# Optimization experiments

Measured on AMD Instinct MI355X. Metric: run time of the kernel, lower is better.

Reference implementation:

```python
import jax, jax.numpy as jnp
import numpy as np

N_HEADS = 32
N_KV_HEADS = 8
THETA = 10000.0


def _rope_tables(head_dim, seq_len):
    # freqs: [head_dim//2]
    freqs = 1.0 / (THETA ** (jnp.arange(0, head_dim, 2, dtype=jnp.float32) / head_dim))
    ang = jnp.arange(seq_len, dtype=jnp.float32)[:, None] * freqs[None, :]  # [T, hd/2]
    return jnp.cos(ang), jnp.sin(ang)


def _apply_rope(x, cos, sin):
    # x: [B, T, H, hd]; cos/sin: [T, hd/2] -> broadcast [1, T, 1, hd/2]
    x_even = x[..., 0::2]
    x_odd = x[..., 1::2]
    c = cos[None, :, None, :]
    s = sin[None, :, None, :]
    out_even = x_even * c - x_odd * s
    out_odd = x_even * s + x_odd * c
    # interleave back to [..., hd]
    out = jnp.stack([out_even, out_odd], axis=-1)
    return out.reshape(x.shape)


def setup_inputs() -> dict:
    key = jax.random.key(0)
    ks = jax.random.split(key, 5)
    B, T, C = 2, 2048, 2048
    kv_dim = (C // N_HEADS) * N_KV_HEADS  # 512
    sc = 1.0 / np.sqrt(C)
    return {
        "x": jax.random.normal(ks[0], (B, T, C), dtype=jnp.float32),
        "wq": jax.random.normal(ks[1], (C, C), dtype=jnp.float32) * sc,
        "wk": jax.random.normal(ks[2], (C, kv_dim), dtype=jnp.float32) * sc,
        "wv": jax.random.normal(ks[3], (C, kv_dim), dtype=jnp.float32) * sc,
        "wo": jax.random.normal(ks[4], (C, C), dtype=jnp.float32) * sc,
    }


def reference(x, wq, wk, wv, wo):
    B, T, C = x.shape
    hd = C // N_HEADS
    rep = N_HEADS // N_KV_HEADS

    q = (x @ wq).reshape(B, T, N_HEADS, hd)
    k = (x @ wk).reshape(B, T, N_KV_HEADS, hd)
    v = (x @ wv).reshape(B, T, N_KV_HEADS, hd)

    cos, sin = _rope_tables(hd, T)
    q = _apply_rope(q, cos, sin)
    k = _apply_rope(k, cos, sin)

    q = q.transpose(0, 2, 1, 3)  # [B, H, T, hd]
    k = k.transpose(0, 2, 1, 3)  # [B, KV, T, hd]
    v = v.transpose(0, 2, 1, 3)

    # GQA: repeat_interleave kv heads to match q heads
    k = jnp.repeat(k, rep, axis=1)
    v = jnp.repeat(v, rep, axis=1)

    scores = jnp.einsum("bhtd,bhsd->bhts", q, k) / jnp.sqrt(jnp.float32(hd))
    weights = jax.nn.softmax(scores, axis=-1)  # no causal mask, as in source
    out = jnp.einsum("bhts,bhsd->bhtd", weights, v)
    out = out.transpose(0, 2, 1, 3).reshape(B, T, C)
    return out @ wo
```

## Files before the change

### kernel.cpp

```cpp
#include <hip/hip_runtime.h>
#include <hip/hip_bf16.h>


typedef unsigned short u16;
typedef short bf16x8 __attribute__((ext_vector_type(8)));
typedef float f32x4 __attribute__((ext_vector_type(4)));
typedef unsigned uint32x4 __attribute__((ext_vector_type(4)));

#define LOG2E 1.4426950408889634f
#define NFREQ (-13.287712379549449f / 32.f)

#if __has_builtin(__builtin_amdgcn_exp2f)
#define EXP2F(x) __builtin_amdgcn_exp2f(x)
#else
#define EXP2F(x) exp2f(x)
#endif

__device__ __forceinline__ float bf2f(u16 u) {
    union { unsigned v; float f; } x; x.v = ((unsigned)u) << 16; return x.f;
}
__device__ __forceinline__ u16 f2bf(float f) {
    unsigned u = __float_as_uint(f);
    u += 0x7fffu + ((u >> 16) & 1u);
    return (u16)(u >> 16);
}
__device__ __forceinline__ unsigned cvt_pk_bf16(float lo, float hi) {
    unsigned r;
    asm("v_cvt_pk_bf16_f32 %0, %1, %2" : "=v"(r) : "v"(lo), "v"(hi));
    return r;
}

__device__ __forceinline__ void async_copy16(const void* g, void* l) {
    __builtin_amdgcn_global_load_lds((const __attribute__((address_space(1))) void*)g,
                                     (__attribute__((address_space(3))) void*)l, 16, 0, 0);
}

#define MFMA16(d, a, b) d = __builtin_amdgcn_mfma_f32_16x16x32_bf16(a, b, d, 0, 0, 0)

__global__ void prep_kernel(const float* __restrict__ x,
                            const float* __restrict__ wq, const float* __restrict__ wk,
                            const float* __restrict__ wv, const float* __restrict__ wo,
                            u16* __restrict__ xbf, u16* __restrict__ wqkvT,
                            u16* __restrict__ woT, float2* __restrict__ rtab) {
    const int bz = blockIdx.z;
    if (bz < 4) {
        const int K = 2048;
        const float* W; u16* Wt; int N;
        switch (bz) {
            case 0:  W = wq; Wt = wqkvT;                        N = 2048; break;
            case 1:  W = wk; Wt = wqkvT + (size_t)2048 * 2048;  N = 512;  break;
            case 2:  W = wv; Wt = wqkvT + (size_t)2560 * 2048;  N = 512;  break;
            default: W = wo; Wt = woT;                          N = 2048; break;
        }
        if ((int)blockIdx.x * 32 >= N) return;
        __shared__ float tile[32][33];
        int xx = blockIdx.x * 32 + threadIdx.x;
        int y0 = blockIdx.y * 32 + threadIdx.y;
        #pragma unroll
        for (int r = 0; r < 32; r += 8)
            tile[threadIdx.y + r][threadIdx.x] = W[(size_t)(y0 + r) * N + xx];
        __syncthreads();
        int xo = blockIdx.y * 32 + threadIdx.x;
        int yo0 = blockIdx.x * 32 + threadIdx.y;
        #pragma unroll
        for (int r = 0; r < 32; r += 8)
            Wt[(size_t)(yo0 + r) * K + xo] = f2bf(tile[threadIdx.x][threadIdx.y + r]);
    } else if (bz == 4) {
        int bid = blockIdx.y * gridDim.x + blockIdx.x;
        int tid = threadIdx.y * 32 + threadIdx.x;
        const size_t n4 = (size_t)4096 * 2048 / 4;
        for (size_t i = (size_t)bid * 256 + tid; i < n4; i += (size_t)4096 * 256) {
            float4 v = ((const float4*)x)[i];
            ushort4 o;
            o.x = f2bf(v.x); o.y = f2bf(v.y); o.z = f2bf(v.z); o.w = f2bf(v.w);
            ((ushort4*)xbf)[i] = o;
        }
    } else {
        int bid = blockIdx.y * gridDim.x + blockIdx.x;
        int idx = bid * 256 + threadIdx.y * 32 + threadIdx.x;
        if (idx < 2048 * 32) {
            int t = idx >> 5, i = idx & 31;
            float freq = exp2f((float)i * NFREQ);
            float s, c;
            sincosf((float)t * freq, &s, &c);
            rtab[idx] = make_float2(c, s);
        }
    }
}

__global__ __launch_bounds__(512) void gemm_qkv_kernel(const u16* __restrict__ A,
                                                       const u16* __restrict__ Bt,
                                                       u16* __restrict__ qout,
                                                       u16* __restrict__ kout,
                                                       u16* __restrict__ vtout,
                                                       const float2* __restrict__ rope_tab,
                                                       int N, int K) {
    __shared__ __align__(16) u16 As[2][16384];
    __shared__ __align__(16) u16 Bs[2][16384];

    const int tid = threadIdx.x;
    const int nwgx = N >> 8;
    const int nwg = 16 * nwgx;
    const int wg = blockIdx.x;
    const int swz = (wg & 7) * (nwg >> 3) + (wg >> 3);
    const int m0 = (swz / nwgx) << 8;
    const int n0 = (swz % nwgx) << 8;

    const int w = tid >> 6, lane = tid & 63, quad = lane >> 4, ln = lane & 15;
    const int wm = w >> 2, wn = w & 3;

    int ldo[2], r128[2], cg8[2];
    #pragma unroll
    for (int p = 0; p < 2; p++) {
        int chunk = p * 512 + tid;
        r128[p] = chunk >> 3;
        cg8[p] = ((chunk & 7) ^ ((chunk >> 3) & 7)) << 3;
        ldo[p] = chunk << 3;
    }
    const u16* pA[2][2]; const u16* pB[2][2];
    #pragma unroll
    for (int h = 0; h < 2; h++)
        #pragma unroll
        for (int p = 0; p < 2; p++) {
            pA[h][p] = A  + (size_t)(m0 + h * 128 + r128[p]) * K + cg8[p];
            pB[h][p] = Bt + (size_t)(n0 + h * 128 + r128[p]) * K + cg8[p];
        }

#define STAGE_A(h, buf) { async_copy16(pA[h][0], &As[buf][(h) * 8192 + ldo[0]]); pA[h][0] += 64; \
                          async_copy16(pA[h][1], &As[buf][(h) * 8192 + ldo[1]]); pA[h][1] += 64; }
#define STAGE_B(h, buf) { async_copy16(pB[h][0], &Bs[buf][(h) * 8192 + ldo[0]]); pB[h][0] += 64; \
                          async_copy16(pB[h][1], &Bs[buf][(h) * 8192 + ldo[1]]); pB[h][1] += 64; }

    f32x4 acc[2][2][4][2];
    #pragma unroll
    for (int mh = 0; mh < 2; mh++)
        #pragma unroll
        for (int nh = 0; nh < 2; nh++)
            #pragma unroll
            for (int i = 0; i < 4; i++)
                #pragma unroll
                for (int j = 0; j < 2; j++)
                    acc[mh][nh][i][j] = (f32x4){0.f, 0.f, 0.f, 0.f};

    STAGE_A(0, 0); STAGE_B(0, 0); STAGE_B(1, 0); STAGE_A(1, 0);
    asm volatile("s_waitcnt vmcnt(4)" ::: "memory");
    __builtin_amdgcn_s_barrier();

    const int nt = K >> 6;
    bf16x8 a[2][4], b0[2][2], b1[2][2];
    const int clq0 = quad ^ (ln & 7), clq1 = (4 + quad) ^ (ln & 7);

    for (int t = 0; t < nt - 1; ++t) {
        const int cur = t & 1, nxt = cur ^ 1;
        const u16* AsC = As[cur];
        const u16* BsC = Bs[cur];
        #pragma unroll
        for (int i = 0; i < 4; i++) {
            int r = wm * 64 + i * 16 + ln;
            a[0][i] = *(const bf16x8*)(&AsC[r * 64 + clq0 * 8]);
            a[1][i] = *(const bf16x8*)(&AsC[r * 64 + clq1 * 8]);
        }
        #pragma unroll
        for (int j = 0; j < 2; j++) {
            int r = wn * 32 + j * 16 + ln;
            b0[0][j] = *(const bf16x8*)(&BsC[r * 64 + clq0 * 8]);
            b0[1][j] = *(const bf16x8*)(&BsC[r * 64 + clq1 * 8]);
        }
        STAGE_A(0, nxt);
        asm volatile("s_waitcnt vmcnt(4)" ::: "memory");
        __builtin_amdgcn_s_barrier();
        __builtin_amdgcn_s_setprio(1);
        #pragma unroll
        for (int kk = 0; kk < 2; kk++)
            #pragma unroll
            for (int i = 0; i < 4; i++)
                #pragma unroll
                for (int j = 0; j < 2; j++)
                    MFMA16(acc[0][0][i][j], a[kk][i], b0[kk][j]);
        __builtin_amdgcn_s_setprio(0);
        __builtin_amdgcn_s_barrier();
        #pragma unroll
        for (int j = 0; j < 2; j++) {
            int r = 128 + wn * 32 + j * 16 + ln;
            b1[0][j] = *(const bf16x8*)(&BsC[r * 64 + clq0 * 8]);
            b1[1][j] = *(const bf16x8*)(&BsC[r * 64 + clq1 * 8]);
        }
        STAGE_B(0, nxt);
        asm volatile("s_waitcnt vmcnt(4)" ::: "memory");
        __builtin_amdgcn_s_barrier();
        __builtin_amdgcn_s_setprio(1);
        #pragma unroll
        for (int kk = 0; kk < 2; kk++)
            #pragma unroll
            for (int i = 0; i < 4; i++)
                #pragma unroll
                for (int j = 0; j < 2; j++)
                    MFMA16(acc[0][1][i][j], a[kk][i], b1[kk][j]);
        __builtin_amdgcn_s_setprio(0);
        __builtin_amdgcn_s_barrier();
        #pragma unroll
        for (int i = 0; i < 4; i++) {
            int r = 128 + wm * 64 + i * 16 + ln;
            a[0][i] = *(const bf16x8*)(&AsC[r * 64 + clq0 * 8]);
            a[1][i] = *(const bf16x8*)(&AsC[r * 64 + clq1 * 8]);
        }
        STAGE_B(1, nxt);
        asm volatile("s_waitcnt vmcnt(4)" ::: "memory");
        __builtin_amdgcn_s_barrier();
        __builtin_amdgcn_s_setprio(1);
        #pragma unroll
        for (int kk = 0; kk < 2; kk++)
            #pragma unroll
            for (int i = 0; i < 4; i++)
                #pragma unroll
                for (int j = 0; j < 2; j++)
                    MFMA16(acc[1][0][i][j], a[kk][i], b0[kk][j]);
        __builtin_amdgcn_s_setprio(0);
        __builtin_amdgcn_s_barrier();
        STAGE_A(1, nxt);
        asm volatile("s_waitcnt vmcnt(4)" ::: "memory");
        __builtin_amdgcn_s_barrier();
        __builtin_amdgcn_s_setprio(1);
        #pragma unroll
        for (int kk = 0; kk < 2; kk++)
            #pragma unroll
            for (int i = 0; i < 4; i++)
                #pragma unroll
                for (int j = 0; j < 2; j++)
                    MFMA16(acc[1][1][i][j], a[kk][i], b1[kk][j]);
        __builtin_amdgcn_s_setprio(0);
        __builtin_amdgcn_s_barrier();
    }

    asm volatile("s_waitcnt vmcnt(0)" ::: "memory");
    __builtin_amdgcn_s_barrier();
    {
        const u16* AsC = As[(nt - 1) & 1];
        const u16* BsC = Bs[(nt - 1) & 1];
        #pragma unroll
        for (int mh = 0; mh < 2; mh++) {
            #pragma unroll
            for (int i = 0; i < 4; i++) {
                int r = mh * 128 + wm * 64 + i * 16 + ln;
                a[0][i] = *(const bf16x8*)(&AsC[r * 64 + clq0 * 8]);
                a[1][i] = *(const bf16x8*)(&AsC[r * 64 + clq1 * 8]);
            }
            #pragma unroll
            for (int nh = 0; nh < 2; nh++) {
                bf16x8 bb[2][2];
                #pragma unroll
                for (int j = 0; j < 2; j++) {
                    int r = nh * 128 + wn * 32 + j * 16 + ln;
                    bb[0][j] = *(const bf16x8*)(&BsC[r * 64 + clq0 * 8]);
                    bb[1][j] = *(const bf16x8*)(&BsC[r * 64 + clq1 * 8]);
                }
                #pragma unroll
                for (int kk = 0; kk < 2; kk++)
                    #pragma unroll
                    for (int i = 0; i < 4; i++)
                        #pragma unroll
                        for (int j = 0; j < 2; j++)
                            MFMA16(acc[mh][nh][i][j], a[kk][i], bb[kk][j]);
            }
        }
    }
#undef STAGE_A
#undef STAGE_B

    if (n0 >= 2560) {
        #pragma unroll
        for (int mh = 0; mh < 2; mh++)
            #pragma unroll
            for (int i = 0; i < 4; i++) {
                int cb = mh * 128 + wm * 64 + i * 16 + quad * 4;
                int sp = (cb & 128) | (cb & 96) | ((cb & 12) << 1) | ((cb & 16) >> 2);
                #pragma unroll
                for (int nh = 0; nh < 2; nh++)
                    #pragma unroll
                    for (int j = 0; j < 2; j++) {
                        int d = n0 + nh * 128 + wn * 32 + j * 16 + ln - 2560;
                        ushort4 o;
                        o.x = f2bf(acc[mh][nh][i][j][0]); o.y = f2bf(acc[mh][nh][i][j][1]);
                        o.z = f2bf(acc[mh][nh][i][j][2]); o.w = f2bf(acc[mh][nh][i][j][3]);
                        *(ushort4*)(&vtout[(size_t)d * 4096 + m0 + sp]) = o;
                    }
            }
        return;
    }
    u16* dst; int ldc, coff; float scale = 1.f;
    if (n0 < 2048) { dst = qout; ldc = 2048; coff = 0;    scale = 0.125f * LOG2E; }
    else           { dst = kout; ldc = 512;  coff = 2048; }
    float fsin = (ln & 1) ? 1.f : -1.f;
    #pragma unroll
    for (int mh = 0; mh < 2; mh++)
        #pragma unroll
        for (int i = 0; i < 4; i++)
            #pragma unroll
            for (int rr = 0; rr < 4; rr++) {
                int row = m0 + mh * 128 + wm * 64 + i * 16 + quad * 4 + rr;
                const float2* trow = rope_tab + (size_t)(row & 2047) * 32;
                #pragma unroll
                for (int nh = 0; nh < 2; nh++)
                    #pragma unroll
                    for (int j = 0; j < 2; j++) {
                        int col = n0 + nh * 128 + wn * 32 + j * 16 + ln;
                        float v = acc[mh][nh][i][j][rr];
                        float p = __shfl_xor(v, 1, 64);
                        float2 cs = trow[(col & 63) >> 1];
                        float rr2 = (v * cs.x + fsin * p * cs.y) * scale;
                        dst[(size_t)row * ldc + col - coff] = f2bf(rr2);
                    }
            }
}

__global__ __launch_bounds__(512) void gemm_out_kernel(const u16* __restrict__ A,
                                                       const u16* __restrict__ Bt,
                                                       float* __restrict__ fC,
                                                       int N, int K) {
    __shared__ __align__(16) u16 As[2][16384];
    __shared__ __align__(16) u16 Bs[2][8192];

    const int tid = threadIdx.x;
    const int nbx = N >> 7;
    const int nwg = 16 * nbx;
    const int wg = blockIdx.x;
    const int swz = (wg & 7) * (nwg >> 3) + (wg >> 3);
    const int m0 = (swz / nbx) << 8;
    const int n0 = (swz % nbx) << 7;

    const int w = tid >> 6, lane = tid & 63, quad = lane >> 4, ln = lane & 15;
    const int wm = w >> 2, wn = w & 3;

    int ldoA[2], rA[2], cgA[2];
    #pragma unroll
    for (int p = 0; p < 2; p++) {
        int chunk = p * 512 + tid;
        rA[p] = chunk >> 3;
        cgA[p] = ((chunk & 7) ^ ((chunk >> 3) & 7)) << 3;
        ldoA[p] = chunk << 3;
    }
    const int rB = tid >> 3;
    const int cgB = ((tid & 7) ^ (rB & 7)) << 3;
    const int ldoB = tid << 3;

    const u16* pA[2][2]; const u16* pB[2];
    #pragma unroll
    for (int h = 0; h < 2; h++) {
        #pragma unroll
        for (int p = 0; p < 2; p++)
            pA[h][p] = A + (size_t)(m0 + h * 128 + rA[p]) * K + cgA[p];
        pB[h] = Bt + (size_t)(n0 + h * 64 + rB) * K + cgB;
    }

#define STAGE_A(h, buf) { async_copy16(pA[h][0], &As[buf][(h) * 8192 + ldoA[0]]); pA[h][0] += 64; \
                          async_copy16(pA[h][1], &As[buf][(h) * 8192 + ldoA[1]]); pA[h][1] += 64; }
#define STAGE_B(h, buf) { async_copy16(pB[h], &Bs[buf][(h) * 4096 + ldoB]); pB[h] += 64; }

    f32x4 acc[2][2][4];
    #pragma unroll
    for (int mh = 0; mh < 2; mh++)
        #pragma unroll
        for (int nh = 0; nh < 2; nh++)
            #pragma unroll
            for (int i = 0; i < 4; i++)
                acc[mh][nh][i] = (f32x4){0.f, 0.f, 0.f, 0.f};

    STAGE_A(0, 0); STAGE_B(0, 0); STAGE_B(1, 0); STAGE_A(1, 0);
    asm volatile("s_waitcnt vmcnt(3)" ::: "memory");
    __builtin_amdgcn_s_barrier();

    const int nt = K >> 6;
    bf16x8 a[2][4], bb0[2], bb1[2];
    const int clq0 = quad ^ (ln & 7), clq1 = (4 + quad) ^ (ln & 7);

    for (int t = 0; t < nt - 1; ++t) {
        const int cur = t & 1, nxt = cur ^ 1;
        const u16* AsC = As[cur];
        const u16* BsC = Bs[cur];
        #pragma unroll
        for (int i = 0; i < 4; i++) {
            int r = wm * 64 + i * 16 + ln;
            a[0][i] = *(const bf16x8*)(&AsC[r * 64 + clq0 * 8]);
            a[1][i] = *(const bf16x8*)(&AsC[r * 64 + clq1 * 8]);
        }
        {
            int r = wn * 16 + ln;
            bb0[0] = *(const bf16x8*)(&BsC[r * 64 + clq0 * 8]);
            bb0[1] = *(const bf16x8*)(&BsC[r * 64 + clq1 * 8]);
        }
        STAGE_A(0, nxt);
        asm volatile("s_waitcnt vmcnt(4)" ::: "memory");
        __builtin_amdgcn_s_barrier();
        __builtin_amdgcn_s_setprio(1);
        #pragma unroll
        for (int kk = 0; kk < 2; kk++)
            #pragma unroll
            for (int i = 0; i < 4; i++)
                MFMA16(acc[0][0][i], a[kk][i], bb0[kk]);
        __builtin_amdgcn_s_setprio(0);
        __builtin_amdgcn_s_barrier();
        {
            int r = wn * 16 + ln;
            bb1[0] = *(const bf16x8*)(&BsC[4096 + r * 64 + clq0 * 8]);
            bb1[1] = *(const bf16x8*)(&BsC[4096 + r * 64 + clq1 * 8]);
        }
        STAGE_B(0, nxt);
        asm volatile("s_waitcnt vmcnt(3)" ::: "memory");
        __builtin_amdgcn_s_barrier();
        __builtin_amdgcn_s_setprio(1);
        #pragma unroll
        for (int kk = 0; kk < 2; kk++)
            #pragma unroll
            for (int i = 0; i < 4; i++)
                MFMA16(acc[0][1][i], a[kk][i], bb1[kk]);
        __builtin_amdgcn_s_setprio(0);
        __builtin_amdgcn_s_barrier();
        #pragma unroll
        for (int i = 0; i < 4; i++) {
            int r = 128 + wm * 64 + i * 16 + ln;
            a[0][i] = *(const bf16x8*)(&AsC[r * 64 + clq0 * 8]);
            a[1][i] = *(const bf16x8*)(&AsC[r * 64 + clq1 * 8]);
        }
        STAGE_B(1, nxt);
        asm volatile("s_waitcnt vmcnt(4)" ::: "memory");
        __builtin_amdgcn_s_barrier();
        __builtin_amdgcn_s_setprio(1);
        #pragma unroll
        for (int kk = 0; kk < 2; kk++)
            #pragma unroll
            for (int i = 0; i < 4; i++)
                MFMA16(acc[1][0][i], a[kk][i], bb0[kk]);
        __builtin_amdgcn_s_setprio(0);
        __builtin_amdgcn_s_barrier();
        STAGE_A(1, nxt);
        asm volatile("s_waitcnt vmcnt(3)" ::: "memory");
        __builtin_amdgcn_s_barrier();
        __builtin_amdgcn_s_setprio(1);
        #pragma unroll
        for (int kk = 0; kk < 2; kk++)
            #pragma unroll
            for (int i = 0; i < 4; i++)
                MFMA16(acc[1][1][i], a[kk][i], bb1[kk]);
        __builtin_amdgcn_s_setprio(0);
        __builtin_amdgcn_s_barrier();
    }

    asm volatile("s_waitcnt vmcnt(0)" ::: "memory");
    __builtin_amdgcn_s_barrier();
    {
        const u16* AsC = As[(nt - 1) & 1];
        const u16* BsC = Bs[(nt - 1) & 1];
        #pragma unroll
        for (int mh = 0; mh < 2; mh++) {
            #pragma unroll
            for (int i = 0; i < 4; i++) {
                int r = mh * 128 + wm * 64 + i * 16 + ln;
                a[0][i] = *(const bf16x8*)(&AsC[r * 64 + clq0 * 8]);
                a[1][i] = *(const bf16x8*)(&AsC[r * 64 + clq1 * 8]);
            }
            #pragma unroll
            for (int nh = 0; nh < 2; nh++) {
                bf16x8 bb[2];
                int r = wn * 16 + ln;
                bb[0] = *(const bf16x8*)(&BsC[nh * 4096 + r * 64 + clq0 * 8]);
                bb[1] = *(const bf16x8*)(&BsC[nh * 4096 + r * 64 + clq1 * 8]);
                #pragma unroll
                for (int kk = 0; kk < 2; kk++)
                    #pragma unroll
                    for (int i = 0; i < 4; i++)
                        MFMA16(acc[mh][nh][i], a[kk][i], bb[kk]);
            }
        }
    }
#undef STAGE_A
#undef STAGE_B

    #pragma unroll
    for (int mh = 0; mh < 2; mh++)
        #pragma unroll
        for (int i = 0; i < 4; i++)
            #pragma unroll
            for (int rr = 0; rr < 4; rr++) {
                int row = m0 + mh * 128 + wm * 64 + i * 16 + quad * 4 + rr;
                #pragma unroll
                for (int nh = 0; nh < 2; nh++) {
                    int col = n0 + nh * 64 + wn * 16 + ln;
                    fC[(size_t)row * N + col] = acc[mh][nh][i][rr];
                }
            }
}

__global__ __launch_bounds__(256) void attn_kernel(const u16* __restrict__ qb,
                                                   const u16* __restrict__ kb,
                                                   const u16* __restrict__ vtb,
                                                   u16* __restrict__ ob) {
    const int T = 2048;
    const int CQ = 2048, CKV = 512;
    __shared__ __align__(16) u16 Ks[2][128 * 64];
    __shared__ __align__(16) u16 Vt[2][64 * 128];

    const int tid = threadIdx.x;
    const int bh = blockIdx.y;
    const int b = bh >> 5, h = bh & 31, kvh = h >> 2;
    const int t0 = blockIdx.x * 128;
    const u16* qbase = qb + ((size_t)(b * T + t0) * CQ + h * 64);
    const u16* kbase = kb + ((size_t)(b * T) * CKV + kvh * 64);
    const u16* vtbase = vtb + ((size_t)(kvh * 64)) * 4096 + b * 2048;

    const int w = tid >> 6, lane = tid & 63, quad = lane >> 4, ln = lane & 15;

    bf16x8 ones;
    #pragma unroll
    for (int e = 0; e < 8; e++) ones[e] = (short)0x3F80;

    const u16* kp[4]; const u16* vp[4];
    int chunks[4];
    #pragma unroll
    for (int p = 0; p < 4; p++) {
        int chunk = p * 256 + tid;
        chunks[p] = chunk;
        int r = chunk >> 3, cl = chunk & 7;
        int cg = cl ^ (r & 7);
        kp[p] = kbase + (size_t)r * CKV + cg * 8;
        int d = chunk >> 4, cl2 = chunk & 15;
        int cg2 = cl2 ^ (d & 7);
        vp[p] = vtbase + (size_t)d * 4096 + cg2 * 8;
    }

    bf16x8 qf[2][2];
    #pragma unroll
    for (int i = 0; i < 2; i++)
        #pragma unroll
        for (int kk = 0; kk < 2; kk++)
            qf[i][kk] = *(const bf16x8*)(&qbase[(size_t)(w * 32 + i * 16 + ln) * CQ + kk * 32 + quad * 8]);

    f32x4 o_acc[2][4];
    f32x4 l_acc[2];
    #pragma unroll
    for (int i = 0; i < 2; i++) {
        l_acc[i] = (f32x4){0.f, 0.f, 0.f, 0.f};
        #pragma unroll
        for (int j = 0; j < 4; j++) o_acc[i][j] = (f32x4){0.f, 0.f, 0.f, 0.f};
    }
    const f32x4 zero4 = (f32x4){0.f, 0.f, 0.f, 0.f};

    #pragma unroll
    for (int p = 0; p < 4; p++) {
        async_copy16(kp[p], &Ks[0][chunks[p] * 8]);
        async_copy16(vp[p], &Vt[0][chunks[p] * 8]);
        kp[p] += 128 * CKV;
        vp[p] += 128;
    }
    __syncthreads();

    int cur = 0;
    for (int st = 0; st < T; st += 128) {
        if (st + 128 < T) {
            #pragma unroll
            for (int p = 0; p < 4; p++) {
                async_copy16(kp[p], &Ks[cur ^ 1][chunks[p] * 8]);
                async_copy16(vp[p], &Vt[cur ^ 1][chunks[p] * 8]);
                kp[p] += 128 * CKV;
                vp[p] += 128;
            }
        }
        const u16* KsC = Ks[cur];
        const u16* VtC = Vt[cur];

        f32x4 s_acc[8][2];
        {
            bf16x8 kf[8];
            #pragma unroll
            for (int j = 0; j < 8; j++) {
                int r = j * 16 + ln;
                int cl = quad ^ (ln & 7);
                kf[j] = *(const bf16x8*)(&KsC[r * 64 + cl * 8]);
            }
            __builtin_amdgcn_s_setprio(1);
            #pragma unroll
            for (int j = 0; j < 8; j++)
                #pragma unroll
                for (int i = 0; i < 2; i++)
                    s_acc[j][i] = __builtin_amdgcn_mfma_f32_16x16x32_bf16(kf[j], qf[i][0], zero4, 0, 0, 0);
            __builtin_amdgcn_s_setprio(0);
        }
        {
            bf16x8 kf[8];
            #pragma unroll
            for (int j = 0; j < 8; j++) {
                int r = j * 16 + ln;
                int cl = (4 + quad) ^ (ln & 7);
                kf[j] = *(const bf16x8*)(&KsC[r * 64 + cl * 8]);
            }
            __builtin_amdgcn_s_setprio(1);
            #pragma unroll
            for (int j = 0; j < 8; j++)
                #pragma unroll
                for (int i = 0; i < 2; i++)
                    s_acc[j][i] = __builtin_amdgcn_mfma_f32_16x16x32_bf16(kf[j], qf[i][1], s_acc[j][i], 0, 0, 0);
            __builtin_amdgcn_s_setprio(0);
        }

        bf16x8 pa[2][4];
        #pragma unroll
        for (int i = 0; i < 2; i++)
            #pragma unroll
            for (int c = 0; c < 4; c++) {
                unsigned w0 = cvt_pk_bf16(EXP2F(s_acc[2 * c][i][0]),     EXP2F(s_acc[2 * c][i][1]));
                unsigned w1 = cvt_pk_bf16(EXP2F(s_acc[2 * c][i][2]),     EXP2F(s_acc[2 * c][i][3]));
                unsigned w2 = cvt_pk_bf16(EXP2F(s_acc[2 * c + 1][i][0]), EXP2F(s_acc[2 * c + 1][i][1]));
                unsigned w3 = cvt_pk_bf16(EXP2F(s_acc[2 * c + 1][i][2]), EXP2F(s_acc[2 * c + 1][i][3]));
                union { uint32x4 u; bf16x8 b; } pu;
                pu.u = (uint32x4){w0, w1, w2, w3};
                pa[i][c] = pu.b;
            }

        #pragma unroll
        for (int c = 0; c < 4; c++) {
            bf16x8 vb[4];
            #pragma unroll
            for (int jd = 0; jd < 4; jd++) {
                int d = jd * 16 + ln;
                int cg = c * 4 + quad;
                int cl = (cg & 8) | ((cg ^ (d & 7)) & 7);
                vb[jd] = *(const bf16x8*)(&VtC[d * 128 + cl * 8]);
            }
            __builtin_amdgcn_s_setprio(1);
            #pragma unroll
            for (int i = 0; i < 2; i++) {
                l_acc[i] = __builtin_amdgcn_mfma_f32_16x16x32_bf16(pa[i][c], ones, l_acc[i], 0, 0, 0);
                #pragma unroll
                for (int jd = 0; jd < 4; jd++)
                    o_acc[i][jd] = __builtin_amdgcn_mfma_f32_16x16x32_bf16(pa[i][c], vb[jd], o_acc[i][jd], 0, 0, 0);
            }
            __builtin_amdgcn_s_setprio(0);
        }

        __syncthreads();
        cur ^= 1;
    }

    #pragma unroll
    for (int i = 0; i < 2; i++)
        #pragma unroll
        for (int rr = 0; rr < 4; rr++) {
            float linv = 1.f / l_acc[i][rr];
            int row = w * 32 + i * 16 + quad * 4 + rr;
            #pragma unroll
            for (int jd = 0; jd < 4; jd++) {
                int col = jd * 16 + ln;
                ob[(size_t)(b * T + t0 + row) * CQ + h * 64 + col] = f2bf(o_acc[i][jd][rr] * linv);
            }
        }
}

#define WS_X_BF   ((size_t)0)
#define WS_WQKVT  ((size_t)16777216)
#define WS_WOT    ((size_t)29360128)
#define WS_QBF    ((size_t)37748736)
#define WS_KBF    ((size_t)54525952)
#define WS_VTBF   ((size_t)58720256)
#define WS_ABF    ((size_t)62914560)

extern "C" void kernel_launch(void* const* d_in, const int* in_sizes, int n_in,
                              void* d_out, int out_size, void* d_ws, size_t ws_size,
                              hipStream_t stream) {
    const float* x  = (const float*)d_in[0];
    const float* wq = (const float*)d_in[1];
    const float* wk = (const float*)d_in[2];
    const float* wv = (const float*)d_in[3];
    const float* wo = (const float*)d_in[4];
    char* ws = (char*)d_ws;
    u16* xbf   = (u16*)(ws + WS_X_BF);
    u16* wqkvT = (u16*)(ws + WS_WQKVT);
    u16* woT   = (u16*)(ws + WS_WOT);
    u16* qbf   = (u16*)(ws + WS_QBF);
    u16* kbf   = (u16*)(ws + WS_KBF);
    u16* vtbf  = (u16*)(ws + WS_VTBF);
    u16* abf   = (u16*)(ws + WS_ABF);
    float2* rtab = (float2*)(ws + WS_ABF);
    float* out = (float*)d_out;

    prep_kernel<<<dim3(64, 64, 6), dim3(32, 8), 0, stream>>>(x, wq, wk, wv, wo,
                                                             xbf, wqkvT, woT, rtab);

    gemm_qkv_kernel<<<dim3(192), 512, 0, stream>>>(xbf, wqkvT, qbf, kbf, vtbf, rtab,
                                                   3072, 2048);

    attn_kernel<<<dim3(16, 64), 256, 0, stream>>>(qbf, kbf, vtbf, abf);

    gemm_out_kernel<<<dim3(256), 512, 0, stream>>>(abf, woT, out, 2048, 2048);
}
```

Before: 289.5 us.

## Widen attention query tile to 256 rows and vectorize weight transpose

The attention kernel now runs 512 threads (8 waves) per block and covers 256 query rows instead of 128. Each double-buffered K/V tile is therefore shared by twice as many queries, which halves global K/V traffic per query, but the grid shrinks to 512 blocks. The prep kernel's weight transpose moves to 64x64 tiles that read with float4 loads, convert to bf16 before staging in shared memory, and write ushort4 vectors. The prep grid is shrunk to match, and the x-conversion loop stride is adjusted to the new block count.

```diff
diff --git a/kernel.cpp b/kernel.cpp
--- a/kernel.cpp
+++ b/kernel.cpp
@@ -43,6 +43,7 @@
                             u16* __restrict__ xbf, u16* __restrict__ wqkvT,
                             u16* __restrict__ woT, float2* __restrict__ rtab) {
     const int bz = blockIdx.z;
+    const int tid = threadIdx.y * 32 + threadIdx.x;
     if (bz < 4) {
         const int K = 2048;
         const float* W; u16* Wt; int N;
@@ -52,24 +53,32 @@
             case 2:  W = wv; Wt = wqkvT + (size_t)2560 * 2048;  N = 512;  break;
             default: W = wo; Wt = woT;                          N = 2048; break;
         }
-        if ((int)blockIdx.x * 32 >= N) return;
-        __shared__ float tile[32][33];
-        int xx = blockIdx.x * 32 + threadIdx.x;
-        int y0 = blockIdx.y * 32 + threadIdx.y;
-        #pragma unroll
-        for (int r = 0; r < 32; r += 8)
-            tile[threadIdx.y + r][threadIdx.x] = W[(size_t)(y0 + r) * N + xx];
+        const int x0 = blockIdx.x * 64;
+        if (x0 >= N) return;
+        const int y0 = blockIdx.y * 64;
+        __shared__ u16 tileT[64][68];
+        const int c4 = tid & 15;
+        #pragma unroll
+        for (int pass = 0; pass < 4; ++pass) {
+            int r = pass * 16 + (tid >> 4);
+            float4 v = *(const float4*)&W[(size_t)(y0 + r) * N + x0 + c4 * 4];
+            tileT[c4 * 4 + 0][r] = f2bf(v.x);
+            tileT[c4 * 4 + 1][r] = f2bf(v.y);
+            tileT[c4 * 4 + 2][r] = f2bf(v.z);
+            tileT[c4 * 4 + 3][r] = f2bf(v.w);
+        }
         __syncthreads();
-        int xo = blockIdx.y * 32 + threadIdx.x;
-        int yo0 = blockIdx.x * 32 + threadIdx.y;
-        #pragma unroll
-        for (int r = 0; r < 32; r += 8)
-            Wt[(size_t)(yo0 + r) * K + xo] = f2bf(tile[threadIdx.x][threadIdx.y + r]);
+        const int rq = tid & 15;
+        #pragma unroll
+        for (int pass = 0; pass < 4; ++pass) {
+            int oc = pass * 16 + (tid >> 4);
+            ushort4 o = *(const ushort4*)&tileT[oc][rq * 4];
+            *(ushort4*)&Wt[(size_t)(x0 + oc) * K + y0 + rq * 4] = o;
+        }
     } else if (bz == 4) {
         int bid = blockIdx.y * gridDim.x + blockIdx.x;
-        int tid = threadIdx.y * 32 + threadIdx.x;
         const size_t n4 = (size_t)4096 * 2048 / 4;
-        for (size_t i = (size_t)bid * 256 + tid; i < n4; i += (size_t)4096 * 256) {
+        for (size_t i = (size_t)bid * 256 + tid; i < n4; i += (size_t)1024 * 256) {
             float4 v = ((const float4*)x)[i];
             ushort4 o;
             o.x = f2bf(v.x); o.y = f2bf(v.y); o.z = f2bf(v.z); o.w = f2bf(v.w);
@@ -77,7 +86,7 @@
         }
     } else {
         int bid = blockIdx.y * gridDim.x + blockIdx.x;
-        int idx = bid * 256 + threadIdx.y * 32 + threadIdx.x;
+        int idx = bid * 256 + tid;
         if (idx < 2048 * 32) {
             int t = idx >> 5, i = idx & 31;
             float freq = exp2f((float)i * NFREQ);
@@ -490,7 +499,7 @@
             }
 }
 
-__global__ __launch_bounds__(256) void attn_kernel(const u16* __restrict__ qb,
+__global__ __launch_bounds__(512) void attn_kernel(const u16* __restrict__ qb,
                                                    const u16* __restrict__ kb,
                                                    const u16* __restrict__ vtb,
                                                    u16* __restrict__ ob) {
@@ -502,7 +511,7 @@
     const int tid = threadIdx.x;
     const int bh = blockIdx.y;
     const int b = bh >> 5, h = bh & 31, kvh = h >> 2;
-    const int t0 = blockIdx.x * 128;
+    const int t0 = blockIdx.x * 256;
     const u16* qbase = qb + ((size_t)(b * T + t0) * CQ + h * 64);
     const u16* kbase = kb + ((size_t)(b * T) * CKV + kvh * 64);
     const u16* vtbase = vtb + ((size_t)(kvh * 64)) * 4096 + b * 2048;
@@ -513,11 +522,11 @@
     #pragma unroll
     for (int e = 0; e < 8; e++) ones[e] = (short)0x3F80;
 
-    const u16* kp[4]; const u16* vp[4];
-    int chunks[4];
-    #pragma unroll
-    for (int p = 0; p < 4; p++) {
-        int chunk = p * 256 + tid;
+    const u16* kp[2]; const u16* vp[2];
+    int chunks[2];
+    #pragma unroll
+    for (int p = 0; p < 2; p++) {
+        int chunk = p * 512 + tid;
         chunks[p] = chunk;
         int r = chunk >> 3, cl = chunk & 7;
         int cg = cl ^ (r & 7);
@@ -545,7 +554,7 @@
     const f32x4 zero4 = (f32x4){0.f, 0.f, 0.f, 0.f};
 
     #pragma unroll
-    for (int p = 0; p < 4; p++) {
+    for (int p = 0; p < 2; p++) {
         async_copy16(kp[p], &Ks[0][chunks[p] * 8]);
         async_copy16(vp[p], &Vt[0][chunks[p] * 8]);
         kp[p] += 128 * CKV;
@@ -557,7 +566,7 @@
     for (int st = 0; st < T; st += 128) {
         if (st + 128 < T) {
             #pragma unroll
-            for (int p = 0; p < 4; p++) {
+            for (int p = 0; p < 2; p++) {
                 async_copy16(kp[p], &Ks[cur ^ 1][chunks[p] * 8]);
                 async_copy16(vp[p], &Vt[cur ^ 1][chunks[p] * 8]);
                 kp[p] += 128 * CKV;
@@ -681,13 +690,13 @@
     float2* rtab = (float2*)(ws + WS_ABF);
     float* out = (float*)d_out;
 
-    prep_kernel<<<dim3(64, 64, 6), dim3(32, 8), 0, stream>>>(x, wq, wk, wv, wo,
+    prep_kernel<<<dim3(32, 32, 6), dim3(32, 8), 0, stream>>>(x, wq, wk, wv, wo,
                                                              xbf, wqkvT, woT, rtab);
 
     gemm_qkv_kernel<<<dim3(192), 512, 0, stream>>>(xbf, wqkvT, qbf, kbf, vtbf, rtab,
                                                    3072, 2048);
 
-    attn_kernel<<<dim3(16, 64), 256, 0, stream>>>(qbf, kbf, vtbf, abf);
+    attn_kernel<<<dim3(8, 64), 512, 0, stream>>>(qbf, kbf, vtbf, abf);
 
     gemm_out_kernel<<<dim3(256), 512, 0, stream>>>(abf, woT, out, 2048, 2048);
 }
```

New measurement: 294.1 us. Within noise of the previous version (+1.6%).
